# Optimization experiments

Measured on AMD Instinct MI355X. Metric: run time of the kernel, lower is better.

The kernel has to match this reference:

```python
import jax, jax.numpy as jnp
import numpy as np

EPS = 1e-5

def _subsys_level(x, W, b, g, beta):
    # x: [S,B,I], W: [S,O,I]  -> Linear -> Tanh -> BatchNorm(batch stats over B)
    h = jnp.einsum('sbi,soi->sbo', x, W) + b[:, None, :]
    h = jnp.tanh(h)
    mu = jnp.mean(h, axis=1, keepdims=True)
    var = jnp.var(h, axis=1, keepdims=True)
    return g[:, None, :] * (h - mu) * jax.lax.rsqrt(var + EPS) + beta[:, None, :]

def setup_inputs() -> dict:
    key = jax.random.key(0)
    ks = jax.random.split(key, 16)
    B, N = 4096, 6000
    u = lambda k, shp: jax.random.uniform(k, shp, jnp.float32, -0.001, 0.001)
    return {
        'mutant_state': jax.random.uniform(ks[0], (B, N), jnp.float32),
        'gene_idx': jax.random.randint(ks[1], (512, 16), 0, N),
        'W1': u(ks[2], (512, 20, 16)), 'b1': u(ks[3], (512, 20)),
        'g1': jnp.ones((512, 20), jnp.float32), 'beta1': jnp.zeros((512, 20), jnp.float32),
        'W2': u(ks[4], (64, 24, 160)), 'b2': u(ks[5], (64, 24)),
        'g2': jnp.ones((64, 24), jnp.float32), 'beta2': jnp.zeros((64, 24), jnp.float32),
        'W3': u(ks[6], (8, 32, 192)), 'b3': u(ks[7], (8, 32)),
        'g3': jnp.ones((8, 32), jnp.float32), 'beta3': jnp.zeros((8, 32), jnp.float32),
        'Wr': u(ks[8], (64, 256)), 'br': u(ks[9], (64,)),
        'gr': jnp.ones((64,), jnp.float32), 'betar': jnp.zeros((64,), jnp.float32),
    }

def reference(mutant_state, gene_idx, W1, b1, g1, beta1, W2, b2, g2, beta2,
              W3, b3, g3, beta3, Wr, br, gr, betar):
    B = mutant_state.shape[0]
    # Level 1 (leaves): gather per-term gene mutant states -> [S1,B,G]
    x1 = jnp.transpose(mutant_state[:, gene_idx], (1, 0, 2))  # [512,B,16]
    o1 = _subsys_level(x1, W1, b1, g1, beta1)                  # [512,B,20]
    # Level 2: each of 64 parents concatenates 8 children outputs -> [64,B,160]
    x2 = o1.reshape(64, 8, B, 20).transpose(0, 2, 1, 3).reshape(64, B, 160)
    o2 = _subsys_level(x2, W2, b2, g2, beta2)                  # [64,B,24]
    # Level 3: 8 parents x 8 children -> [8,B,192]
    x3 = o2.reshape(8, 8, B, 24).transpose(0, 2, 1, 3).reshape(8, B, 192)
    o3 = _subsys_level(x3, W3, b3, g3, beta3)                  # [8,B,32]
    # Root: concat 8 outputs -> [B,256]
    xr = o3.transpose(1, 0, 2).reshape(B, 256)
    hr = jnp.tanh(xr @ Wr.T + br)
    mu = jnp.mean(hr, axis=0, keepdims=True)
    var = jnp.var(hr, axis=0, keepdims=True)
    return gr * (hr - mu) * jax.lax.rsqrt(var + EPS) + betar  # [B,64]
```

## Files before the change

kernel.cpp:

```cpp
#include <hip/hip_runtime.h>
#include <hip/hip_fp16.h>

#define BATCH 4096
#define EPS 1e-5f

typedef __half h16;
typedef float f32x2 __attribute__((ext_vector_type(2)));
typedef _Float16 h16x2 __attribute__((ext_vector_type(2)));
typedef unsigned int u32;

union H8 { float4 f4; h16 h[8]; __half2 h2[4]; };
union U4 { float4 f4; u32 u[4]; };
union H2U { float f; __half2 h2; h16x2 hv; u32 u; };

__device__ __forceinline__ float tanh_fast(float x){
  float e = __expf(2.0f*x);
  return 1.0f - 2.0f*__builtin_amdgcn_rcpf(e + 1.0f);
}

__device__ __forceinline__ float wred(float v){
  #pragma unroll
  for (int off=32; off; off>>=1) v += __shfl_xor(v, off);
  return v;
}

__device__ __forceinline__ float dot2(u32 a, u32 b, float c){
#if __has_builtin(__builtin_amdgcn_fdot2)
  H2U ua, ub; ua.u = a; ub.u = b;
  return __builtin_amdgcn_fdot2(ua.hv, ub.hv, c, false);
#else
  H2U ua, ub; ua.u = a; ub.u = b;
  float2 fa = __half22float2(ua.h2);
  float2 fb = __half22float2(ub.h2);
  return fmaf(fa.y, fb.y, fmaf(fa.x, fb.x, c));
#endif
}

__global__ __launch_bounds__(256) void k_transpose(const float* __restrict__ ms, h16* __restrict__ msT){
  __shared__ float tile[64][65];
  int tc = blockIdx.x * 64;
  int tb = blockIdx.y * 64;
  int tx = threadIdx.x & 63;
  int ty = threadIdx.x >> 6;
  #pragma unroll
  for (int k=0;k<16;++k){
    int r = ty + k*4;
    int c = tc + tx;
    if (c < 6000) tile[r][tx] = ms[(size_t)(tb + r)*6000 + c];
  }
  __syncthreads();
  #pragma unroll
  for (int k=0;k<16;++k){
    int r = ty + k*4;
    int c = tc + r;
    if (c < 6000) msT[(size_t)c*BATCH + tb + tx] = __float2half(tile[tx][r]);
  }
}

__global__ __launch_bounds__(64,2) void k_statsA(const h16* __restrict__ msT, const int* __restrict__ gidx,
    const float* __restrict__ W1, const float* __restrict__ b1,
    u32* __restrict__ H1p, float* __restrict__ part1){
  const int s = blockIdx.y;
  const int bc = blockIdx.x;
  const int lane = threadIdx.x;
  const int b0 = bc*512 + lane*8;
  const float* Wp = W1 + s*320;
  f32x2 acc[20][4];
  #pragma unroll
  for (int o=0;o<20;++o){
    float bv = b1[s*20+o];
    #pragma unroll
    for (int k=0;k<4;++k) acc[o][k] = (f32x2){bv,bv};
  }
  #pragma unroll 4
  for (int g=0; g<16; ++g){
    const int row = gidx[s*16+g]*BATCH;
    H8 u; u.f4 = *reinterpret_cast<const float4*>(msT + row + b0);
    f32x2 x[4];
    #pragma unroll
    for (int k=0;k<4;++k){
      float2 f = __half22float2(u.h2[k]);
      x[k] = (f32x2){f.x, f.y};
    }
    #pragma unroll
    for (int o=0;o<20;++o){
      float wv = Wp[o*16+g];
      f32x2 w2 = (f32x2){wv,wv};
      #pragma unroll
      for (int k=0;k<4;++k) acc[o][k] = __builtin_elementwise_fma(x[k], w2, acc[o][k]);
    }
  }
  #pragma unroll
  for (int op=0;op<10;++op){
    const int oA = 2*op, oB = 2*op+1;
    float hA[8], hB[8];
    #pragma unroll
    for (int k=0;k<4;++k){
      hA[2*k]   = tanh_fast(acc[oA][k].x);
      hA[2*k+1] = tanh_fast(acc[oA][k].y);
      hB[2*k]   = tanh_fast(acc[oB][k].x);
      hB[2*k+1] = tanh_fast(acc[oB][k].y);
    }
    U4 v0, v1;
    #pragma unroll
    for (int k=0;k<4;++k){
      H2U a; a.h2 = __halves2half2(__float2half(hA[k]),   __float2half(hB[k]));   v0.u[k] = a.u;
      H2U b; b.h2 = __halves2half2(__float2half(hA[k+4]), __float2half(hB[k+4])); v1.u[k] = b.u;
    }
    u32* dst = H1p + (size_t)(s*10+op)*BATCH + b0;
    *reinterpret_cast<float4*>(dst)     = v0.f4;
    *reinterpret_cast<float4*>(dst + 4) = v1.f4;
    float SA = ((hA[0]+hA[1])+(hA[2]+hA[3])) + ((hA[4]+hA[5])+(hA[6]+hA[7]));
    float QA = ((hA[0]*hA[0]+hA[1]*hA[1])+(hA[2]*hA[2]+hA[3]*hA[3]))
             + ((hA[4]*hA[4]+hA[5]*hA[5])+(hA[6]*hA[6]+hA[7]*hA[7]));
    float SB = ((hB[0]+hB[1])+(hB[2]+hB[3])) + ((hB[4]+hB[5])+(hB[6]+hB[7]));
    float QB = ((hB[0]*hB[0]+hB[1]*hB[1])+(hB[2]*hB[2]+hB[3]*hB[3]))
             + ((hB[4]*hB[4]+hB[5]*hB[5])+(hB[6]*hB[6]+hB[7]*hB[7]));
    SA = wred(SA); QA = wred(QA); SB = wred(SB); QB = wred(QB);
    if (lane==0){
      part1[((s*20+oA)*2  )*8 + bc] = SA;
      part1[((s*20+oA)*2+1)*8 + bc] = QA;
      part1[((s*20+oB)*2  )*8 + bc] = SB;
      part1[((s*20+oB)*2+1)*8 + bc] = QB;
    }
  }
}

__global__ __launch_bounds__(256) void k_fold2(const float* __restrict__ W, const float* __restrict__ bb,
    const float* __restrict__ g, const float* __restrict__ beta,
    const float* __restrict__ part, u32* __restrict__ W2h, float* __restrict__ bf){
  const int p = blockIdx.x;
  const int tid = threadIdx.x;
  __shared__ float aL[160], cL[160];
  for (int t = tid; t < 160; t += 256){
    int ch = p*160 + t;
    float S=0.f, Q=0.f;
    for (int bc=0; bc<8; ++bc){ S += part[(ch*2)*8 + bc]; Q += part[(ch*2+1)*8 + bc]; }
    float mu  = S * (1.0f/BATCH);
    float var = Q * (1.0f/BATCH) - mu*mu;
    float a = g[ch] * rsqrtf(var + EPS);
    aL[t] = a;
    cL[t] = beta[ch] - a*mu;
  }
  __syncthreads();
  const int NW = 160*24;
  for (int e = tid; e < 80*24; e += 256){
    int i2 = e / 24, j = e % 24;
    float w0 = W[p*NW + j*160 + 2*i2    ] * aL[2*i2];
    float w1 = W[p*NW + j*160 + 2*i2 + 1] * aL[2*i2+1];
    H2U u; u.h2 = __halves2half2(__float2half(w0), __float2half(w1));
    W2h[p*1920 + e] = u.u;
  }
  if (tid < 24){
    float sv = bb[p*24 + tid];
    for (int i=0;i<160;++i) sv = fmaf(W[p*NW + tid*160 + i], cL[i], sv);
    bf[p*24 + tid] = sv;
  }
}

__global__ __launch_bounds__(512) void k_passB(const u32* __restrict__ H1p,
    const u32* __restrict__ W2h, const float* __restrict__ b2f,
    h16* __restrict__ H2){
  const int p = blockIdx.y;
  const int bc = blockIdx.x;
  const int tid = threadIdx.x;
  const int b = bc*512 + tid;
  float acc[24];
  #pragma unroll
  for (int j=0;j<24;++j) acc[j] = b2f[p*24+j];
  const u32* __restrict__ wp = W2h + p*1920;
  const u32* __restrict__ hbase = H1p + (size_t)p*80*BATCH + b;
  u32 buf[2][10];
  #pragma unroll
  for (int op=0;op<10;++op) buf[0][op] = hbase[(size_t)op*BATCH];
  #pragma unroll
  for (int c=0;c<8;++c){
    if (c < 7){
      #pragma unroll
      for (int op=0;op<10;++op)
        buf[(c+1)&1][op] = hbase[(size_t)((c+1)*10+op)*BATCH];
    }
    const u32* wj0 = wp + c*240;
    #pragma unroll
    for (int op=0;op<10;++op){
      const u32 xa = buf[c&1][op];
      const u32* wj = wj0 + op*24;
      #pragma unroll
      for (int j=0;j<24;++j){
        acc[j] = dot2(xa, wj[j], acc[j]);
      }
    }
  }
  float v[24];
  #pragma unroll
  for (int j=0;j<24;++j) v[j] = tanh_fast(acc[j]);
  h16* dst = H2 + ((size_t)p*BATCH + b)*24;
  #pragma unroll
  for (int t=0;t<3;++t){
    H8 u;
    #pragma unroll
    for (int k=0;k<8;++k) u.h[k] = __float2half(v[t*8+k]);
    *reinterpret_cast<float4*>(dst + t*8) = u.f4;
  }
}

__global__ __launch_bounds__(256) void k_stats2(const h16* __restrict__ H2, float* __restrict__ part2){
  const int p = blockIdx.y;
  const int bc = blockIdx.x;
  const int tid = threadIdx.x;
  const int wv = tid >> 6;
  const int lane = tid & 63;
  float S[24], Q[24];
  #pragma unroll
  for (int j=0;j<24;++j){ S[j]=0.f; Q[j]=0.f; }
  const h16* base = H2 + ((size_t)p*BATCH + bc*1024 + tid)*24;
  for (int it=0; it<4; ++it){
    const h16* src = base + (size_t)it*256*24;
    #pragma unroll
    for (int t=0;t<3;++t){
      H8 u; u.f4 = *reinterpret_cast<const float4*>(src + t*8);
      #pragma unroll
      for (int i=0;i<8;++i){
        float v = __half2float(u.h[i]);
        S[t*8+i] += v;
        Q[t*8+i] = fmaf(v, v, Q[t*8+i]);
      }
    }
  }
  __shared__ float red[2][4][24];
  #pragma unroll
  for (int j=0;j<24;++j){
    float s = wred(S[j]);
    float q = wred(Q[j]);
    if (lane==0){ red[0][wv][j] = s; red[1][wv][j] = q; }
  }
  __syncthreads();
  if (tid < 24){
    float s = (red[0][0][tid]+red[0][1][tid]) + (red[0][2][tid]+red[0][3][tid]);
    float q = (red[1][0][tid]+red[1][1][tid]) + (red[1][2][tid]+red[1][3][tid]);
    const int ch = p*24 + tid;
    part2[(ch*2  )*4 + bc] = s;
    part2[(ch*2+1)*4 + bc] = q;
  }
}

__global__ __launch_bounds__(512) void k_passC(const h16* __restrict__ H2, const float* __restrict__ part2,
    const float* __restrict__ g2, const float* __restrict__ beta2,
    const float* __restrict__ W3, const float* __restrict__ b3,
    h16* __restrict__ H3, float* __restrict__ part3){
  const int q = blockIdx.y;
  const int bc = blockIdx.x;
  const int tid = threadIdx.x;
  const int wv = tid >> 6;
  const int lane = tid & 63;
  __shared__ float aL[192], cL[192];
  for (int t = tid; t < 192; t += 512){
    int ch = q*192 + t;
    float S=0.f, Q=0.f;
    #pragma unroll
    for (int c=0;c<4;++c){ S += part2[(ch*2)*4 + c]; Q += part2[(ch*2+1)*4 + c]; }
    float mu  = S * (1.0f/BATCH);
    float var = Q * (1.0f/BATCH) - mu*mu;
    float a = g2[ch] * rsqrtf(var + EPS);
    aL[t] = a; cL[t] = beta2[ch] - a*mu;
  }
  __syncthreads();
  const int b = bc*64 + lane;
  const int jb = wv*4;
  float acc[4];
  #pragma unroll
  for (int j=0;j<4;++j) acc[j] = b3[q*32 + jb + j];
  for (int c2=0;c2<8;++c2){
    const h16* src = H2 + ((size_t)(q*8+c2)*BATCH + b)*24;
    float xn[24];
    #pragma unroll
    for (int t=0;t<3;++t){
      H8 u; u.f4 = *reinterpret_cast<const float4*>(src + t*8);
      #pragma unroll
      for (int i=0;i<8;++i){
        int ci = c2*24 + t*8 + i;
        xn[t*8+i] = fmaf(aL[ci], __half2float(u.h[i]), cL[ci]);
      }
    }
    #pragma unroll
    for (int j=0;j<4;++j){
      const float* wr = W3 + q*6144 + (jb+j)*192 + c2*24;
      #pragma unroll
      for (int i=0;i<24;++i) acc[j] = fmaf(xn[i], wr[i], acc[j]);
    }
  }
  #pragma unroll
  for (int j=0;j<4;++j) acc[j] = tanh_fast(acc[j]);
  {
    h16* dst = H3 + (size_t)b*256 + q*32 + jb;
    H2U u0,u1;
    u0.h2 = __halves2half2(__float2half(acc[0]), __float2half(acc[1]));
    u1.h2 = __halves2half2(__float2half(acc[2]), __float2half(acc[3]));
    float2 vv; vv.x = u0.f; vv.y = u1.f;
    *reinterpret_cast<float2*>(dst) = vv;
  }
  #pragma unroll
  for (int j=0;j<4;++j){
    float S = wred(acc[j]);
    float Q = wred(acc[j]*acc[j]);
    if (lane==0){
      part3[((q*32+jb+j)*2  )*64 + bc] = S;
      part3[((q*32+jb+j)*2+1)*64 + bc] = Q;
    }
  }
}

__global__ __launch_bounds__(256) void k_passD(const h16* __restrict__ H3, const float* __restrict__ part3,
    const float* __restrict__ g3, const float* __restrict__ beta3,
    const float* __restrict__ Wr, const float* __restrict__ br,
    float* __restrict__ Hr, float* __restrict__ partR){
  const int bc = blockIdx.x;
  const int jb = blockIdx.y * 8;
  const int tid = threadIdx.x;
  const int wv = tid >> 6;
  const int lane = tid & 63;
  __shared__ float aL[256], cL[256];
  __shared__ float lacc[4][64][9];
  {
    float S=0.f, Q=0.f;
    for (int c=0;c<64;++c){ S += part3[(tid*2)*64 + c]; Q += part3[(tid*2+1)*64 + c]; }
    float mu  = S * (1.0f/BATCH);
    float var = Q * (1.0f/BATCH) - mu*mu;
    float a = g3[tid] * rsqrtf(var + EPS);
    aL[tid] = a; cL[tid] = beta3[tid] - a*mu;
  }
  __syncthreads();
  const int b = bc*64 + lane;
  float acc[8];
  #pragma unroll
  for (int j=0;j<8;++j) acc[j] = 0.f;
  const h16* src = H3 + (size_t)b*256 + wv*64;
  #pragma unroll
  for (int kk=0; kk<8; ++kk){
    const int sl = wv*8 + kk;
    H8 u; u.f4 = *reinterpret_cast<const float4*>(src + kk*8);
    float xn[8];
    #pragma unroll
    for (int i=0;i<8;++i){
      int ci = sl*8+i;
      xn[i] = fmaf(aL[ci], __half2float(u.h[i]), cL[ci]);
    }
    #pragma unroll
    for (int j=0;j<8;++j){
      const float* wr = Wr + (jb+j)*256 + sl*8;
      #pragma unroll
      for (int i=0;i<8;++i) acc[j] = fmaf(xn[i], wr[i], acc[j]);
    }
  }
  #pragma unroll
  for (int j=0;j<8;++j) lacc[wv][lane][j] = acc[j];
  __syncthreads();
  #pragma unroll
  for (int k=0;k<2;++k){
    const int j = k*4 + wv;
    float v = br[jb+j] + (lacc[0][lane][j] + lacc[1][lane][j]) + (lacc[2][lane][j] + lacc[3][lane][j]);
    v = tanh_fast(v);
    Hr[(size_t)b*64 + jb + j] = v;
    float S = wred(v);
    float Q = wred(v*v);
    if (lane==0){
      partR[((jb+j)*2  )*64 + bc] = S;
      partR[((jb+j)*2+1)*64 + bc] = Q;
    }
  }
}

__global__ __launch_bounds__(256) void k_final(const float* __restrict__ Hr, const float* __restrict__ partR,
    const float* __restrict__ gr, const float* __restrict__ betar, float* __restrict__ out){
  __shared__ float aL[64], cL[64];
  const int tid = threadIdx.x;
  if (tid < 64){
    float S=0.f, Q=0.f;
    for (int bc=0; bc<64; ++bc){ S += partR[(tid*2)*64 + bc]; Q += partR[(tid*2+1)*64 + bc]; }
    float mu  = S * (1.0f/BATCH);
    float var = Q * (1.0f/BATCH) - mu*mu;
    float a = gr[tid] * rsqrtf(var + EPS);
    aL[tid] = a; cL[tid] = betar[tid] - a*mu;
  }
  __syncthreads();
  const int i4 = blockIdx.x*256 + tid;
  float4 v = *reinterpret_cast<const float4*>(Hr + (size_t)i4*4);
  int o = (i4*4)&63;
  float4 r;
  r.x = aL[o  ]*v.x + cL[o  ];
  r.y = aL[o+1]*v.y + cL[o+1];
  r.z = aL[o+2]*v.z + cL[o+2];
  r.w = aL[o+3]*v.w + cL[o+3];
  *reinterpret_cast<float4*>(out + (size_t)i4*4) = r;
}

extern "C" void kernel_launch(void* const* d_in, const int* in_sizes, int n_in,
                              void* d_out, int out_size, void* d_ws, size_t ws_size,
                              hipStream_t stream) {
  const float* ms    = (const float*)d_in[0];
  const int*   gidx  = (const int*)  d_in[1];
  const float* W1    = (const float*)d_in[2];
  const float* b1    = (const float*)d_in[3];
  const float* g1    = (const float*)d_in[4];
  const float* beta1 = (const float*)d_in[5];
  const float* W2    = (const float*)d_in[6];
  const float* b2    = (const float*)d_in[7];
  const float* g2    = (const float*)d_in[8];
  const float* beta2 = (const float*)d_in[9];
  const float* W3    = (const float*)d_in[10];
  const float* b3    = (const float*)d_in[11];
  const float* g3    = (const float*)d_in[12];
  const float* beta3 = (const float*)d_in[13];
  const float* Wr    = (const float*)d_in[14];
  const float* br    = (const float*)d_in[15];
  const float* gr    = (const float*)d_in[16];
  const float* betar = (const float*)d_in[17];
  float* out = (float*)d_out;

  char* w = (char*)d_ws;
  size_t off = 0;
  auto take = [&](size_t bytes)->char*{
    char* p = w + off;
    off = (off + bytes + 255) & ~(size_t)255;
    return p;
  };
  h16*   msT    = (h16*)  take((size_t)6000*BATCH*2);
  u32*   H1p    = (u32*)  take((size_t)5120*BATCH*4);
  h16*   H2     = (h16*)  take((size_t)64*BATCH*24*2);
  h16*   H3     = (h16*)  take((size_t)BATCH*256*2);
  float* Hr     = (float*)take((size_t)BATCH*64*4);
  float* part1  = (float*)take((size_t)10240*2*8*4);
  float* part2  = (float*)take((size_t)1536*2*4*4);
  float* part3  = (float*)take((size_t)256*2*64*4);
  float* partR  = (float*)take((size_t)64*2*64*4);
  u32*   W2h    = (u32*)  take((size_t)64*1920*4);
  float* b2f    = (float*)take((size_t)64*24*4);
  if (off > ws_size) return;

  k_transpose<<<dim3(94,64), 256, 0, stream>>>(ms, msT);
  k_statsA<<<dim3(8,512), 64, 0, stream>>>(msT, gidx, W1, b1, H1p, part1);
  k_fold2<<<64, 256, 0, stream>>>(W2, b2, g1, beta1, part1, W2h, b2f);
  k_passB<<<dim3(8,64), 512, 0, stream>>>(H1p, W2h, b2f, H2);
  k_stats2<<<dim3(4,64), 256, 0, stream>>>(H2, part2);
  k_passC<<<dim3(64,8), 512, 0, stream>>>(H2, part2, g2, beta2, W3, b3, H3, part3);
  k_passD<<<dim3(64,8), 256, 0, stream>>>(H3, part3, g3, beta3, Wr, br, Hr, partR);
  k_final<<<256, 256, 0, stream>>>(Hr, partR, gr, betar, out);
}
```

Baseline: 181.3 us.

## Compute level-2 linear layer with MFMA 16x16x32 f16 instead of scalar dot2

Level-2 matmul in k_passB moves from per-thread fdot2 accumulation over 24 outputs to MFMA 16x16x32 f16 instructions. k_fold2 now pre-packs the BN-folded weights into MFMA A-fragment layout, zero-padded from 24 to 32 outputs. The H1 activations are staged through padded LDS tiles of 64 batch rows so they can be read as B-fragments, and launch geometry changes to 256-thread blocks with 16 batch chunks. This targets the VALU dot-product cost, but adds LDS staging, syncthreads and padded wasted MFMA work.

```diff
diff --git a/kernel.cpp b/kernel.cpp
--- a/kernel.cpp
+++ b/kernel.cpp
@@ -6,12 +6,14 @@
 
 typedef __half h16;
 typedef float f32x2 __attribute__((ext_vector_type(2)));
-typedef _Float16 h16x2 __attribute__((ext_vector_type(2)));
+typedef float f32x4 __attribute__((ext_vector_type(4)));
+typedef _Float16 half8 __attribute__((ext_vector_type(8)));
 typedef unsigned int u32;
 
 union H8 { float4 f4; h16 h[8]; __half2 h2[4]; };
 union U4 { float4 f4; u32 u[4]; };
-union H2U { float f; __half2 h2; h16x2 hv; u32 u; };
+union H2U { float f; __half2 h2; u32 u; };
+union FRU { uint4 q; half8 h; };
 
 __device__ __forceinline__ float tanh_fast(float x){
   float e = __expf(2.0f*x);
@@ -22,18 +24,6 @@
   #pragma unroll
   for (int off=32; off; off>>=1) v += __shfl_xor(v, off);
   return v;
-}
-
-__device__ __forceinline__ float dot2(u32 a, u32 b, float c){
-#if __has_builtin(__builtin_amdgcn_fdot2)
-  H2U ua, ub; ua.u = a; ub.u = b;
-  return __builtin_amdgcn_fdot2(ua.hv, ub.hv, c, false);
-#else
-  H2U ua, ub; ua.u = a; ub.u = b;
-  float2 fa = __half22float2(ua.h2);
-  float2 fb = __half22float2(ub.h2);
-  return fmaf(fa.y, fb.y, fmaf(fa.x, fb.x, c));
-#endif
 }
 
 __global__ __launch_bounds__(256) void k_transpose(const float* __restrict__ ms, h16* __restrict__ msT){
@@ -128,7 +118,7 @@
 
 __global__ __launch_bounds__(256) void k_fold2(const float* __restrict__ W, const float* __restrict__ bb,
     const float* __restrict__ g, const float* __restrict__ beta,
-    const float* __restrict__ part, u32* __restrict__ W2h, float* __restrict__ bf){
+    const float* __restrict__ part, uint4* __restrict__ Wfrag, float* __restrict__ bf){
   const int p = blockIdx.x;
   const int tid = threadIdx.x;
   __shared__ float aL[160], cL[160];
@@ -143,64 +133,87 @@
     cL[t] = beta[ch] - a*mu;
   }
   __syncthreads();
-  const int NW = 160*24;
-  for (int e = tid; e < 80*24; e += 256){
-    int i2 = e / 24, j = e % 24;
-    float w0 = W[p*NW + j*160 + 2*i2    ] * aL[2*i2];
-    float w1 = W[p*NW + j*160 + 2*i2 + 1] * aL[2*i2+1];
-    H2U u; u.h2 = __halves2half2(__float2half(w0), __float2half(w1));
-    W2h[p*1920 + e] = u.u;
+  for (int E = tid; E < 640; E += 256){
+    int f = E >> 6, l = E & 63;
+    int jt = f/5, kc = f%5;
+    int j = jt*16 + (l&15);
+    int gg = l>>4;
+    u32 q[4];
+    #pragma unroll
+    for (int e2=0; e2<4; ++e2){
+      int i0 = kc*32 + gg*8 + 2*e2;
+      float w0=0.f, w1=0.f;
+      if (j < 24){
+        w0 = W[p*3840 + j*160 + i0    ] * aL[i0];
+        w1 = W[p*3840 + j*160 + i0 + 1] * aL[i0+1];
+      }
+      H2U u; u.h2 = __halves2half2(__float2half(w0), __float2half(w1));
+      q[e2] = u.u;
+    }
+    Wfrag[p*640 + E] = make_uint4(q[0],q[1],q[2],q[3]);
   }
   if (tid < 24){
     float sv = bb[p*24 + tid];
-    for (int i=0;i<160;++i) sv = fmaf(W[p*NW + tid*160 + i], cL[i], sv);
+    for (int i=0;i<160;++i) sv = fmaf(W[p*3840 + tid*160 + i], cL[i], sv);
     bf[p*24 + tid] = sv;
   }
 }
 
-__global__ __launch_bounds__(512) void k_passB(const u32* __restrict__ H1p,
-    const u32* __restrict__ W2h, const float* __restrict__ b2f,
+__global__ __launch_bounds__(256) void k_passB(const u32* __restrict__ H1p,
+    const uint4* __restrict__ Wfrag, const float* __restrict__ b2f,
     h16* __restrict__ H2){
   const int p = blockIdx.y;
   const int bc = blockIdx.x;
   const int tid = threadIdx.x;
-  const int b = bc*512 + tid;
-  float acc[24];
-  #pragma unroll
-  for (int j=0;j<24;++j) acc[j] = b2f[p*24+j];
-  const u32* __restrict__ wp = W2h + p*1920;
-  const u32* __restrict__ hbase = H1p + (size_t)p*80*BATCH + b;
-  u32 buf[2][10];
-  #pragma unroll
-  for (int op=0;op<10;++op) buf[0][op] = hbase[(size_t)op*BATCH];
-  #pragma unroll
-  for (int c=0;c<8;++c){
-    if (c < 7){
-      #pragma unroll
-      for (int op=0;op<10;++op)
-        buf[(c+1)&1][op] = hbase[(size_t)((c+1)*10+op)*BATCH];
-    }
-    const u32* wj0 = wp + c*240;
-    #pragma unroll
-    for (int op=0;op<10;++op){
-      const u32 xa = buf[c&1][op];
-      const u32* wj = wj0 + op*24;
-      #pragma unroll
-      for (int j=0;j<24;++j){
-        acc[j] = dot2(xa, wj[j], acc[j]);
-      }
-    }
-  }
-  float v[24];
-  #pragma unroll
-  for (int j=0;j<24;++j) v[j] = tanh_fast(acc[j]);
-  h16* dst = H2 + ((size_t)p*BATCH + b)*24;
-  #pragma unroll
-  for (int t=0;t<3;++t){
-    H8 u;
-    #pragma unroll
-    for (int k=0;k<8;++k) u.h[k] = __float2half(v[t*8+k]);
-    *reinterpret_cast<float4*>(dst + t*8) = u.f4;
+  const int wv = tid >> 6;
+  const int l = tid & 63;
+  const int g = l >> 4;
+  __shared__ u32 lds[64*84];
+  half8 wf[10];
+  #pragma unroll
+  for (int f=0; f<10; ++f){
+    FRU u; u.q = Wfrag[p*640 + f*64 + l];
+    wf[f] = u.h;
+  }
+  const u32* __restrict__ hp = H1p + (size_t)p*80*BATCH;
+  const float* bp = b2f + p*24;
+  float bj0[4], bj1[4];
+  #pragma unroll
+  for (int r=0;r<4;++r){
+    bj0[r] = bp[g*4+r];
+    bj1[r] = (g<2) ? bp[16+g*4+r] : 0.f;
+  }
+  for (int it=0; it<4; ++it){
+    const int b0 = bc*256 + it*64;
+    __syncthreads();
+    #pragma unroll
+    for (int rr=0; rr<20; ++rr){
+      int r = rr*4 + wv;
+      lds[l*84 + r] = hp[(size_t)r*BATCH + b0 + l];
+    }
+    __syncthreads();
+    const int bb = wv*16 + (l&15);
+    f32x4 acc0 = {0.f,0.f,0.f,0.f}, acc1 = {0.f,0.f,0.f,0.f};
+    #pragma unroll
+    for (int kc=0; kc<5; ++kc){
+      FRU u; u.q = *reinterpret_cast<const uint4*>(&lds[bb*84 + kc*16 + g*4]);
+      acc0 = __builtin_amdgcn_mfma_f32_16x16x32_f16(wf[kc],   u.h, acc0, 0,0,0);
+      acc1 = __builtin_amdgcn_mfma_f32_16x16x32_f16(wf[5+kc], u.h, acc1, 0,0,0);
+    }
+    const int B = b0 + bb;
+    h16* dst = H2 + ((size_t)p*BATCH + B)*24;
+    {
+      H2U u0,u1;
+      u0.h2 = __halves2half2(__float2half(tanh_fast(acc0[0]+bj0[0])), __float2half(tanh_fast(acc0[1]+bj0[1])));
+      u1.h2 = __halves2half2(__float2half(tanh_fast(acc0[2]+bj0[2])), __float2half(tanh_fast(acc0[3]+bj0[3])));
+      *reinterpret_cast<uint2*>(dst + g*4) = make_uint2(u0.u, u1.u);
+    }
+    if (g < 2){
+      H2U u0,u1;
+      u0.h2 = __halves2half2(__float2half(tanh_fast(acc1[0]+bj1[0])), __float2half(tanh_fast(acc1[1]+bj1[1])));
+      u1.h2 = __halves2half2(__float2half(tanh_fast(acc1[2]+bj1[2])), __float2half(tanh_fast(acc1[3]+bj1[3])));
+      *reinterpret_cast<uint2*>(dst + 16 + g*4) = make_uint2(u0.u, u1.u);
+    }
   }
 }
 
@@ -433,14 +446,14 @@
   float* part2  = (float*)take((size_t)1536*2*4*4);
   float* part3  = (float*)take((size_t)256*2*64*4);
   float* partR  = (float*)take((size_t)64*2*64*4);
-  u32*   W2h    = (u32*)  take((size_t)64*1920*4);
+  uint4* Wfrag  = (uint4*)take((size_t)64*640*16);
   float* b2f    = (float*)take((size_t)64*24*4);
   if (off > ws_size) return;
 
   k_transpose<<<dim3(94,64), 256, 0, stream>>>(ms, msT);
   k_statsA<<<dim3(8,512), 64, 0, stream>>>(msT, gidx, W1, b1, H1p, part1);
-  k_fold2<<<64, 256, 0, stream>>>(W2, b2, g1, beta1, part1, W2h, b2f);
-  k_passB<<<dim3(8,64), 512, 0, stream>>>(H1p, W2h, b2f, H2);
+  k_fold2<<<64, 256, 0, stream>>>(W2, b2, g1, beta1, part1, Wfrag, b2f);
+  k_passB<<<dim3(16,64), 256, 0, stream>>>(H1p, Wfrag, b2f, H2);
   k_stats2<<<dim3(4,64), 256, 0, stream>>>(H2, part2);
   k_passC<<<dim3(64,8), 512, 0, stream>>>(H2, part2, g2, beta2, W3, b3, H3, part3);
   k_passD<<<dim3(64,8), 256, 0, stream>>>(H3, part3, g3, beta3, Wr, br, Hr, partR);
```

Measured after the change: 155.9 us (median of 2 runs). 14.0% less time.
